# Kernel tuning notes

Measured on AMD Instinct MI355X. Metric: run time of the kernel, lower is better.

Reference implementation:

```python
import jax, jax.numpy as jnp
import numpy as np

B, T, C, H = 1, 4096, 768, 12
D = C // H  # head_dim = 64


def setup_inputs() -> dict:
    key = jax.random.key(0)
    ks = jax.random.split(key, 5)
    s = 1.0 / np.sqrt(C)
    return {
        "x": jax.random.normal(ks[0], (B, T, C), dtype=jnp.float32),
        "Wq": jax.random.normal(ks[1], (C, C), dtype=jnp.float32) * s,
        "bq": jnp.zeros((C,), dtype=jnp.float32),
        "Wk": jax.random.normal(ks[2], (C, C), dtype=jnp.float32) * s,
        "bk": jnp.zeros((C,), dtype=jnp.float32),
        "Wv": jax.random.normal(ks[3], (C, C), dtype=jnp.float32) * s,
        "bv": jnp.zeros((C,), dtype=jnp.float32),
        "Wo": jax.random.normal(ks[4], (C, C), dtype=jnp.float32) * s,
        "bo": jnp.zeros((C,), dtype=jnp.float32),
    }


def reference(x, Wq, bq, Wk, bk, Wv, bv, Wo, bo):
    # Linear projections (torch nn.Linear: y = x @ W.T + b)
    q = (x @ Wq.T + bq).reshape(B, T, H, D).transpose(0, 2, 1, 3)  # [B,H,T,D]
    k = (x @ Wk.T + bk).reshape(B, T, H, D).transpose(0, 2, 1, 3)
    v = (x @ Wv.T + bv).reshape(B, T, H, D).transpose(0, 2, 1, 3)
    scale = 1.0 / jnp.sqrt(jnp.asarray(D, dtype=x.dtype))
    scores = jnp.einsum("bhqd,bhkd->bhqk", q, k) * scale  # [B,H,T,T]
    attn = jax.nn.softmax(scores, axis=-1)
    out = jnp.einsum("bhqk,bhkd->bhqd", attn, v)  # [B,H,T,D]
    y = out.transpose(0, 2, 1, 3).reshape(B, T, C)
    return y @ Wo.T + bo
```

## Files before the change

### kernel.cpp

```cpp
#include <hip/hip_runtime.h>
#include <math.h>

#define T_ 4096
#define C_ 768
#define H_ 12
#define D_ 64
#define TC_ ((size_t)T_ * C_)
#define CC_ ((size_t)C_ * C_)

typedef __attribute__((ext_vector_type(8))) __bf16 bf16x8;
typedef __attribute__((ext_vector_type(4))) __bf16 bf16x4;
typedef __attribute__((ext_vector_type(2))) __bf16 bf16x2;
typedef __attribute__((ext_vector_type(4))) float f32x4;
typedef __attribute__((ext_vector_type(16))) float f32x16;
typedef __attribute__((ext_vector_type(8))) unsigned short u16x8;

#define MFIX 24.0f

static __device__ __forceinline__ float fast_exp2(float x) {
#if __has_builtin(__builtin_amdgcn_exp2f)
    return __builtin_amdgcn_exp2f(x);
#else
    return exp2f(x);
#endif
}

static __device__ __forceinline__ unsigned pack2(float a, float b) {
    bf16x2 v = { (__bf16)a, (__bf16)b };
    return __builtin_bit_cast(unsigned, v);
}

static __device__ __forceinline__ void gload16(const void* g, void* l) {
    __builtin_amdgcn_global_load_lds(
        (const __attribute__((address_space(1))) unsigned int*)g,
        (__attribute__((address_space(3))) unsigned int*)l, 16, 0, 0);
}

__global__ void f2b_kernel(const float* __restrict__ in,
                           unsigned short* __restrict__ out, int n4) {
    int i = blockIdx.x * blockDim.x + threadIdx.x;
    const int stride = gridDim.x * blockDim.x;
    for (; i < n4; i += stride) {
        float4 v = ((const float4*)in)[i];
        bf16x4 o = { (__bf16)v.x, (__bf16)v.y, (__bf16)v.z, (__bf16)v.w };
        *(bf16x4*)&out[(size_t)i * 4] = o;
    }
}

__global__ void f2b4_kernel(const float* __restrict__ w0, const float* __restrict__ w1,
                            const float* __restrict__ w2, const float* __restrict__ w3,
                            unsigned short* __restrict__ out) {
    const float* src = (blockIdx.y == 0) ? w0 : (blockIdx.y == 1) ? w1
                     : (blockIdx.y == 2) ? w2 : w3;
    unsigned short* dst = out + (size_t)blockIdx.y * CC_;
    const int i = blockIdx.x * blockDim.x + threadIdx.x;
    float4 v = ((const float4*)src)[i];
    bf16x4 o = { (__bf16)v.x, (__bf16)v.y, (__bf16)v.z, (__bf16)v.w };
    *(bf16x4*)&dst[(size_t)i * 4] = o;
}

#define BM 128
#define BN 128
#define BKG 64

struct GemmRegs {
    const unsigned short* ag[4];
    const unsigned short* wg[4];
    unsigned short* la[4];
    unsigned short* lw[4];
    int lq, lg, wr, wc;
};

static __device__ __forceinline__ void gemm_setup(
    GemmRegs& R, const unsigned short* A, const unsigned short* W,
    unsigned short* Asm, unsigned short* Bsm, int bm, int bn, int K)
{
    const int tid = threadIdx.x;
    const int wave = tid >> 6, lane = tid & 63;
    R.lq = lane & 15; R.lg = lane >> 4;
    R.wr = wave >> 1; R.wc = wave & 1;
#pragma unroll
    for (int i = 0; i < 4; ++i) {
        const int flat = wave * 256 + i * 64 + lane;
        const int row = flat >> 3, cb = flat & 7;
        R.ag[i] = A + (size_t)(bm + row) * K + cb * 8;
        R.wg[i] = W + (size_t)(bn + row) * K + cb * 8;
        R.la[i] = Asm + (wave * 4 + i) * 512;
        R.lw[i] = Bsm + (wave * 4 + i) * 512;
    }
}

static __device__ __forceinline__ void gemm_loop(
    GemmRegs& R, unsigned short* Asm, unsigned short* Bsm, int K, f32x4 acc[4][4])
{
    for (int kb = 0; kb < K; kb += BKG) {
        __syncthreads();
#pragma unroll
        for (int i = 0; i < 4; ++i) {
            gload16(R.ag[i] + kb, R.la[i]);
            gload16(R.wg[i] + kb, R.lw[i]);
        }
        __syncthreads();
        __builtin_amdgcn_s_setprio(1);
#pragma unroll
        for (int ks = 0; ks < 2; ++ks) {
            bf16x8 af[4], wf[4];
#pragma unroll
            for (int m = 0; m < 4; ++m)
                af[m] = *(const bf16x8*)&Asm[(R.wr * 64 + m * 16 + R.lq) * BKG + ks * 32 + R.lg * 8];
#pragma unroll
            for (int n = 0; n < 4; ++n)
                wf[n] = *(const bf16x8*)&Bsm[(R.wc * 64 + n * 16 + R.lq) * BKG + ks * 32 + R.lg * 8];
#pragma unroll
            for (int m = 0; m < 4; ++m)
#pragma unroll
                for (int n = 0; n < 4; ++n)
                    acc[m][n] = __builtin_amdgcn_mfma_f32_16x16x32_bf16(af[m], wf[n], acc[m][n], 0, 0, 0);
        }
        __builtin_amdgcn_s_setprio(0);
    }
}

__global__ __launch_bounds__(256) void qkv128(
    const unsigned short* __restrict__ xb,
    const unsigned short* __restrict__ Wqb, const unsigned short* __restrict__ Wkb,
    const unsigned short* __restrict__ Wvb,
    const float* __restrict__ bq, const float* __restrict__ bk, const float* __restrict__ bv,
    unsigned short* __restrict__ Qb, unsigned short* __restrict__ Kb,
    unsigned short* __restrict__ Vtb)
{
    __shared__ unsigned short Asm[BM * BKG];
    __shared__ unsigned short Bsm[BN * BKG];
    const int z = blockIdx.z;
    const unsigned short* W = (z == 0) ? Wqb : (z == 1) ? Wkb : Wvb;
    const float* bias = (z == 0) ? bq : (z == 1) ? bk : bv;
    const int bm = blockIdx.x * BM, bn = blockIdx.y * BN;

    GemmRegs R;
    gemm_setup(R, xb, W, Asm, Bsm, bm, bn, C_);
    f32x4 acc[4][4] = {};
    gemm_loop(R, Asm, Bsm, C_, acc);

    const float sc = (z == 0) ? 0.18033688011112042f : 1.0f;
#pragma unroll
    for (int mt = 0; mt < 4; ++mt) {
        const int m0 = bm + R.wr * 64 + mt * 16 + R.lg * 4;
#pragma unroll
        for (int nt = 0; nt < 4; ++nt) {
            const int n = bn + R.wc * 64 + nt * 16 + R.lq;
            const float b = bias[n];
            if (z == 2) {
                bf16x4 o = { (__bf16)(acc[mt][nt][0] + b), (__bf16)(acc[mt][nt][1] + b),
                             (__bf16)(acc[mt][nt][2] + b), (__bf16)(acc[mt][nt][3] + b) };
                *(bf16x4*)&Vtb[(size_t)n * T_ + m0] = o;
            } else {
                unsigned short* Y = (z == 0) ? Qb : Kb;
#pragma unroll
                for (int r = 0; r < 4; ++r)
                    Y[(size_t)(m0 + r) * C_ + n] =
                        __builtin_bit_cast(unsigned short, (__bf16)((acc[mt][nt][r] + b) * sc));
            }
        }
    }
}

__global__ __launch_bounds__(256) void out128(
    const unsigned short* __restrict__ ctxb, const unsigned short* __restrict__ Wob,
    const float* __restrict__ bo, float* __restrict__ out)
{
    __shared__ unsigned short Asm[BM * BKG];
    __shared__ unsigned short Bsm[BN * BKG];
    const int bm = blockIdx.x * BM, bn = blockIdx.y * BN;

    GemmRegs R;
    gemm_setup(R, ctxb, Wob, Asm, Bsm, bm, bn, C_);
    f32x4 acc[4][4] = {};
    gemm_loop(R, Asm, Bsm, C_, acc);

#pragma unroll
    for (int mt = 0; mt < 4; ++mt) {
        const int m0 = bm + R.wr * 64 + mt * 16 + R.lg * 4;
#pragma unroll
        for (int nt = 0; nt < 4; ++nt) {
            const int n = bn + R.wc * 64 + nt * 16 + R.lq;
            const float b = bo[n];
#pragma unroll
            for (int r = 0; r < 4; ++r)
                out[(size_t)(m0 + r) * C_ + n] = acc[mt][nt][r] + b;
        }
    }
}

#define SPLITS 2
#define KVTILES (T_ / 64 / SPLITS)

__global__ __launch_bounds__(128, 3) void attn32s(
    const unsigned short* __restrict__ Qb, const unsigned short* __restrict__ Kb,
    const unsigned short* __restrict__ Vtb, unsigned short* __restrict__ Opart,
    float* __restrict__ mlpart)
{
    __shared__ unsigned short Ks[64 * 64];
    __shared__ unsigned short Vs[64 * 64];
    __shared__ unsigned short Ps[2][32 * 64];

    const int tid = threadIdx.x;
    const int wave = tid >> 6, lane = tid & 63;
    const int lq = lane & 31, hi = lane >> 5;

    const int bid = blockIdx.x;
    const int sw = (bid & 7) * 192 + (bid >> 3);
    const int split = sw / 768;
    const int rem = sw - split * 768;
    const int h = rem >> 6, qt = rem & 63;
    const int q0 = qt * 64 + wave * 32;
    const int kv0 = split * (T_ / SPLITS);

    const int swz = (lq & 7) << 4;
    int rof[4];
#pragma unroll
    for (int ks = 0; ks < 4; ++ks)
        rof[ks] = lq * 128 + ((hi * 16 + ks * 32) ^ swz);

    bf16x8 qf[4];
    {
        const unsigned short* qp = Qb + (size_t)(q0 + lq) * C_ + h * D_ + hi * 8;
#pragma unroll
        for (int ks = 0; ks < 4; ++ks) qf[ks] = *(const bf16x8*)(qp + ks * 16);
    }

    const int srow = (lane >> 3);
    const int soff = (lane & 7) * 16;
    const char* gkb = (const char*)Kb +
        (size_t)(kv0 + wave * 32 + srow) * (C_ * 2) + h * (D_ * 2) + soff;
    const char* gvb = (const char*)Vtb +
        (size_t)(h * D_ + wave * 32 + srow) * (T_ * 2) + kv0 * 2 + soff;
    char* kds = (char*)Ks + (wave * 32 + srow) * 128 + (soff ^ (srow << 4));
    char* vds = (char*)Vs + (wave * 32 + srow) * 128 + (soff ^ (srow << 4));

    u16x8 kreg[4], vreg[4];
#pragma unroll
    for (int k = 0; k < 4; ++k) {
        kreg[k] = *(const u16x8*)(gkb + k * 8 * (C_ * 2));
        vreg[k] = *(const u16x8*)(gvb + k * 8 * (T_ * 2));
    }

    f32x16 oacc0 = {}, oacc1 = {};
    float lrun = 0.f;

    for (int it = 0; it < KVTILES; ++it) {
        __syncthreads();
#pragma unroll
        for (int k = 0; k < 4; ++k) {
            *(u16x8*)(kds + k * 1024) = kreg[k];
            *(u16x8*)(vds + k * 1024) = vreg[k];
        }
        __syncthreads();

        if (it + 1 < KVTILES) {
            const char* gk = gkb + (size_t)(it + 1) * 64 * (C_ * 2);
            const char* gv = gvb + (size_t)(it + 1) * 128;
#pragma unroll
            for (int k = 0; k < 4; ++k) {
                kreg[k] = *(const u16x8*)(gk + k * 8 * (C_ * 2));
                vreg[k] = *(const u16x8*)(gv + k * 8 * (T_ * 2));
            }
        }

        const char* kb = (const char*)&Ks[0];
        const char* vb = (const char*)&Vs[0];

        f32x16 s0 = {}, s1 = {};
        __builtin_amdgcn_s_setprio(1);
#pragma unroll
        for (int ks = 0; ks < 4; ++ks) {
            bf16x8 kf0 = *(const bf16x8*)(kb + rof[ks]);
            bf16x8 kf1 = *(const bf16x8*)(kb + 4096 + rof[ks]);
            s0 = __builtin_amdgcn_mfma_f32_32x32x16_bf16(kf0, qf[ks], s0, 0, 0, 0);
            s1 = __builtin_amdgcn_mfma_f32_32x32x16_bf16(kf1, qf[ks], s1, 0, 0, 0);
        }
        __builtin_amdgcn_s_setprio(0);

#pragma unroll
        for (int r = 0; r < 16; ++r) {
            s0[r] = fast_exp2(s0[r] - MFIX);
            s1[r] = fast_exp2(s1[r] - MFIX);
        }
        {
            float ps[8];
#pragma unroll
            for (int r = 0; r < 8; ++r)
                ps[r] = (s0[r] + s0[r + 8]) + (s1[r] + s1[r + 8]);
            ps[0] += ps[4]; ps[1] += ps[5]; ps[2] += ps[6]; ps[3] += ps[7];
            float pt = (ps[0] + ps[1]) + (ps[2] + ps[3]);
            lrun += pt + __shfl_xor(pt, 32);
        }

        char* pw = (char*)&Ps[wave][0] + lq * 128;
#pragma unroll
        for (int g = 0; g < 4; ++g) {
            uint2 w0 = { pack2(s0[4 * g + 0], s0[4 * g + 1]),
                         pack2(s0[4 * g + 2], s0[4 * g + 3]) };
            *(uint2*)(pw + ((16 * g) ^ swz) + 8 * hi) = w0;
            uint2 w1 = { pack2(s1[4 * g + 0], s1[4 * g + 1]),
                         pack2(s1[4 * g + 2], s1[4 * g + 3]) };
            *(uint2*)(pw + ((16 * (g + 4)) ^ swz) + 8 * hi) = w1;
        }

        __builtin_amdgcn_s_setprio(1);
#pragma unroll
        for (int ks = 0; ks < 4; ++ks) {
            bf16x8 pf = *(const bf16x8*)((const char*)&Ps[wave][0] + lq * 128 +
                                         (((unsigned)(ks * 32 + hi * 16)) ^ swz));
            bf16x8 vf0 = *(const bf16x8*)(vb + rof[ks]);
            bf16x8 vf1 = *(const bf16x8*)(vb + 4096 + rof[ks]);
            oacc0 = __builtin_amdgcn_mfma_f32_32x32x16_bf16(vf0, pf, oacc0, 0, 0, 0);
            oacc1 = __builtin_amdgcn_mfma_f32_32x32x16_bf16(vf1, pf, oacc1, 0, 0, 0);
        }
        __builtin_amdgcn_s_setprio(0);
    }

    unsigned short* op = Opart + ((size_t)(split * H_ + h) * T_ + q0 + lq) * 64;
#pragma unroll
    for (int k = 0; k < 4; ++k) {
        bf16x4 o0 = { (__bf16)oacc0[4 * k + 0], (__bf16)oacc0[4 * k + 1],
                      (__bf16)oacc0[4 * k + 2], (__bf16)oacc0[4 * k + 3] };
        *(bf16x4*)&op[8 * k + 4 * hi] = o0;
        bf16x4 o1 = { (__bf16)oacc1[4 * k + 0], (__bf16)oacc1[4 * k + 1],
                      (__bf16)oacc1[4 * k + 2], (__bf16)oacc1[4 * k + 3] };
        *(bf16x4*)&op[32 + 8 * k + 4 * hi] = o1;
    }
    if (hi == 0) {
        float2 ml; ml.x = MFIX; ml.y = lrun;
        *(float2*)&mlpart[((size_t)(split * H_ + h) * T_ + q0 + lq) * 2] = ml;
    }
}

__global__ __launch_bounds__(256) void combine2(
    const unsigned short* __restrict__ Opart, const float* __restrict__ mlpart,
    unsigned short* __restrict__ ctxb)
{
    const int idx = blockIdx.x * 256 + threadIdx.x;
    const int dq = idx & 15;
    const int ht = idx >> 4;
    const int h = ht >> 12;
    const int t = ht & (T_ - 1);
    const size_t b0 = (size_t)h * T_ + t;
    const size_t b1 = (size_t)(H_ + h) * T_ + t;
    const float2 ml0 = *(const float2*)&mlpart[b0 * 2];
    const float2 ml1 = *(const float2*)&mlpart[b1 * 2];
    const float m = fmaxf(ml0.x, ml1.x);
    const float w0 = fast_exp2(ml0.x - m);
    const float w1 = fast_exp2(ml1.x - m);
    const float inv = 1.f / (w0 * ml0.y + w1 * ml1.y);
    const bf16x4 a0 = *(const bf16x4*)&Opart[b0 * 64 + dq * 4];
    const bf16x4 a1 = *(const bf16x4*)&Opart[b1 * 64 + dq * 4];
    bf16x4 r;
#pragma unroll
    for (int i = 0; i < 4; ++i)
        r[i] = (__bf16)(((float)a0[i] * w0 + (float)a1[i] * w1) * inv);
    *(bf16x4*)&ctxb[(size_t)t * C_ + h * D_ + dq * 4] = r;
}

extern "C" void kernel_launch(void* const* d_in, const int* in_sizes, int n_in,
                              void* d_out, int out_size, void* d_ws, size_t ws_size,
                              hipStream_t stream) {
    (void)in_sizes; (void)n_in; (void)out_size; (void)ws_size;
    const float* x  = (const float*)d_in[0];
    const float* Wq = (const float*)d_in[1];
    const float* bq = (const float*)d_in[2];
    const float* Wk = (const float*)d_in[3];
    const float* bk = (const float*)d_in[4];
    const float* Wv = (const float*)d_in[5];
    const float* bv = (const float*)d_in[6];
    const float* Wo = (const float*)d_in[7];
    const float* bo = (const float*)d_in[8];
    float* out = (float*)d_out;

    unsigned short* ws    = (unsigned short*)d_ws;
    unsigned short* xb    = ws;
    unsigned short* Wqb   = xb + TC_;
    unsigned short* Wkb   = Wqb + CC_;
    unsigned short* Wvb   = Wkb + CC_;
    unsigned short* Wob   = Wvb + CC_;
    unsigned short* Qb    = Wob + CC_;
    unsigned short* Kb    = Qb + TC_;
    unsigned short* Vtb   = Kb + TC_;
    unsigned short* ctxb  = Vtb + TC_;
    unsigned short* Opart = ctxb + TC_;
    float* mlpart = (float*)(Opart + 2 * TC_);

    f2b_kernel<<<2048, 256, 0, stream>>>(x, xb, (int)(TC_ / 4));
    dim3 gw(CC_ / 4 / 256, 4);
    f2b4_kernel<<<gw, 256, 0, stream>>>(Wq, Wk, Wv, Wo, Wqb);

    dim3 gq(T_ / BM, C_ / BN, 3);
    qkv128<<<gq, 256, 0, stream>>>(xb, Wqb, Wkb, Wvb, bq, bk, bv, Qb, Kb, Vtb);

    attn32s<<<1536, 128, 0, stream>>>(Qb, Kb, Vtb, Opart, mlpart);
    combine2<<<(T_ * H_ * 16) / 256, 256, 0, stream>>>(Opart, mlpart, ctxb);

    dim3 go(T_ / BM, C_ / BN);
    out128<<<go, 256, 0, stream>>>(ctxb, Wob, bo, out);
}
```

Measured before the change: 140.2 us.

## Keep P in registers via lane shuffles and raise attention KV splits to four

The softmax probabilities are repacked into MFMA B-operand fragments with cross-half lane shuffles instead of a round trip through LDS. This drops the Ps shared buffer and raises the occupancy hint from 3 to 5 blocks. The KV dimension is now split four ways when the workspace is large enough, which doubles the grid to 3072 blocks. The combine step sums the split partials directly, since all splits share the fixed max. The extra split adds more partial-output traffic to and from global memory in the combine kernel.

```diff
diff --git a/kernel.cpp b/kernel.cpp
--- a/kernel.cpp
+++ b/kernel.cpp
@@ -14,6 +14,7 @@
 typedef __attribute__((ext_vector_type(4))) float f32x4;
 typedef __attribute__((ext_vector_type(16))) float f32x16;
 typedef __attribute__((ext_vector_type(8))) unsigned short u16x8;
+typedef __attribute__((ext_vector_type(4))) unsigned int u32x4;
 
 #define MFIX 24.0f
 
@@ -191,29 +192,28 @@
     }
 }
 
-#define SPLITS 2
-#define KVTILES (T_ / 64 / SPLITS)
-
-__global__ __launch_bounds__(128, 3) void attn32s(
+template <int SPLITS>
+__global__ __launch_bounds__(128, 5) void attn32s(
     const unsigned short* __restrict__ Qb, const unsigned short* __restrict__ Kb,
     const unsigned short* __restrict__ Vtb, unsigned short* __restrict__ Opart,
-    float* __restrict__ mlpart)
+    float* __restrict__ lpart)
 {
     __shared__ unsigned short Ks[64 * 64];
     __shared__ unsigned short Vs[64 * 64];
-    __shared__ unsigned short Ps[2][32 * 64];
 
     const int tid = threadIdx.x;
     const int wave = tid >> 6, lane = tid & 63;
     const int lq = lane & 31, hi = lane >> 5;
 
+    const int perx = (SPLITS * 768) / 8;
     const int bid = blockIdx.x;
-    const int sw = (bid & 7) * 192 + (bid >> 3);
+    const int sw = (bid & 7) * perx + (bid >> 3);
     const int split = sw / 768;
     const int rem = sw - split * 768;
     const int h = rem >> 6, qt = rem & 63;
     const int q0 = qt * 64 + wave * 32;
     const int kv0 = split * (T_ / SPLITS);
+    const int KVTILES = T_ / 64 / SPLITS;
 
     const int swz = (lq & 7) << 4;
     int rof[4];
@@ -295,26 +295,36 @@
             lrun += pt + __shfl_xor(pt, 32);
         }
 
-        char* pw = (char*)&Ps[wave][0] + lq * 128;
-#pragma unroll
-        for (int g = 0; g < 4; ++g) {
-            uint2 w0 = { pack2(s0[4 * g + 0], s0[4 * g + 1]),
-                         pack2(s0[4 * g + 2], s0[4 * g + 3]) };
-            *(uint2*)(pw + ((16 * g) ^ swz) + 8 * hi) = w0;
-            uint2 w1 = { pack2(s1[4 * g + 0], s1[4 * g + 1]),
-                         pack2(s1[4 * g + 2], s1[4 * g + 3]) };
-            *(uint2*)(pw + ((16 * (g + 4)) ^ swz) + 8 * hi) = w1;
+        bf16x8 pf[4];
+#pragma unroll
+        for (int half = 0; half < 2; ++half) {
+            const f32x16& s = half ? s1 : s0;
+            unsigned g[8];
+#pragma unroll
+            for (int a = 0; a < 8; ++a) g[a] = pack2(s[2 * a], s[2 * a + 1]);
+            unsigned V0 = hi ? g[0] : g[2];
+            unsigned V1 = hi ? g[1] : g[3];
+            unsigned xV0 = __shfl_xor((int)V0, 32);
+            unsigned xV1 = __shfl_xor((int)V1, 32);
+            u32x4 pk0 = { hi ? xV0 : g[0], hi ? xV1 : g[1],
+                          hi ? g[2] : xV0, hi ? g[3] : xV1 };
+            pf[2 * half + 0] = __builtin_bit_cast(bf16x8, pk0);
+            unsigned W0 = hi ? g[4] : g[6];
+            unsigned W1 = hi ? g[5] : g[7];
+            unsigned xW0 = __shfl_xor((int)W0, 32);
+            unsigned xW1 = __shfl_xor((int)W1, 32);
+            u32x4 pk1 = { hi ? xW0 : g[4], hi ? xW1 : g[5],
+                          hi ? g[6] : xW0, hi ? g[7] : xW1 };
+            pf[2 * half + 1] = __builtin_bit_cast(bf16x8, pk1);
         }
 
         __builtin_amdgcn_s_setprio(1);
 #pragma unroll
         for (int ks = 0; ks < 4; ++ks) {
-            bf16x8 pf = *(const bf16x8*)((const char*)&Ps[wave][0] + lq * 128 +
-                                         (((unsigned)(ks * 32 + hi * 16)) ^ swz));
             bf16x8 vf0 = *(const bf16x8*)(vb + rof[ks]);
             bf16x8 vf1 = *(const bf16x8*)(vb + 4096 + rof[ks]);
-            oacc0 = __builtin_amdgcn_mfma_f32_32x32x16_bf16(vf0, pf, oacc0, 0, 0, 0);
-            oacc1 = __builtin_amdgcn_mfma_f32_32x32x16_bf16(vf1, pf, oacc1, 0, 0, 0);
+            oacc0 = __builtin_amdgcn_mfma_f32_32x32x16_bf16(vf0, pf[ks], oacc0, 0, 0, 0);
+            oacc1 = __builtin_amdgcn_mfma_f32_32x32x16_bf16(vf1, pf[ks], oacc1, 0, 0, 0);
         }
         __builtin_amdgcn_s_setprio(0);
     }
@@ -329,14 +339,13 @@
                       (__bf16)oacc1[4 * k + 2], (__bf16)oacc1[4 * k + 3] };
         *(bf16x4*)&op[32 + 8 * k + 4 * hi] = o1;
     }
-    if (hi == 0) {
-        float2 ml; ml.x = MFIX; ml.y = lrun;
-        *(float2*)&mlpart[((size_t)(split * H_ + h) * T_ + q0 + lq) * 2] = ml;
-    }
-}
-
-__global__ __launch_bounds__(256) void combine2(
-    const unsigned short* __restrict__ Opart, const float* __restrict__ mlpart,
+    if (hi == 0)
+        lpart[(size_t)(split * H_ + h) * T_ + q0 + lq] = lrun;
+}
+
+template <int SPLITS>
+__global__ __launch_bounds__(256) void combineS(
+    const unsigned short* __restrict__ Opart, const float* __restrict__ lpart,
     unsigned short* __restrict__ ctxb)
 {
     const int idx = blockIdx.x * 256 + threadIdx.x;
@@ -344,27 +353,30 @@
     const int ht = idx >> 4;
     const int h = ht >> 12;
     const int t = ht & (T_ - 1);
-    const size_t b0 = (size_t)h * T_ + t;
-    const size_t b1 = (size_t)(H_ + h) * T_ + t;
-    const float2 ml0 = *(const float2*)&mlpart[b0 * 2];
-    const float2 ml1 = *(const float2*)&mlpart[b1 * 2];
-    const float m = fmaxf(ml0.x, ml1.x);
-    const float w0 = fast_exp2(ml0.x - m);
-    const float w1 = fast_exp2(ml1.x - m);
-    const float inv = 1.f / (w0 * ml0.y + w1 * ml1.y);
-    const bf16x4 a0 = *(const bf16x4*)&Opart[b0 * 64 + dq * 4];
-    const bf16x4 a1 = *(const bf16x4*)&Opart[b1 * 64 + dq * 4];
+
+    float denom = 0.f;
+#pragma unroll
+    for (int sp = 0; sp < SPLITS; ++sp)
+        denom += lpart[(size_t)(sp * H_ + h) * T_ + t];
+    const float inv = 1.f / denom;
+
+    float acc[4] = {};
+#pragma unroll
+    for (int sp = 0; sp < SPLITS; ++sp) {
+        const bf16x4 a = *(const bf16x4*)&Opart[((size_t)(sp * H_ + h) * T_ + t) * 64 + dq * 4];
+#pragma unroll
+        for (int i = 0; i < 4; ++i) acc[i] += (float)a[i];
+    }
     bf16x4 r;
 #pragma unroll
-    for (int i = 0; i < 4; ++i)
-        r[i] = (__bf16)(((float)a0[i] * w0 + (float)a1[i] * w1) * inv);
+    for (int i = 0; i < 4; ++i) r[i] = (__bf16)(acc[i] * inv);
     *(bf16x4*)&ctxb[(size_t)t * C_ + h * D_ + dq * 4] = r;
 }
 
 extern "C" void kernel_launch(void* const* d_in, const int* in_sizes, int n_in,
                               void* d_out, int out_size, void* d_ws, size_t ws_size,
                               hipStream_t stream) {
-    (void)in_sizes; (void)n_in; (void)out_size; (void)ws_size;
+    (void)in_sizes; (void)n_in; (void)out_size;
     const float* x  = (const float*)d_in[0];
     const float* Wq = (const float*)d_in[1];
     const float* bq = (const float*)d_in[2];
@@ -387,7 +399,10 @@
     unsigned short* Vtb   = Kb + TC_;
     unsigned short* ctxb  = Vtb + TC_;
     unsigned short* Opart = ctxb + TC_;
-    float* mlpart = (float*)(Opart + 2 * TC_);
+
+    const size_t lsz = (size_t)H_ * T_ * sizeof(float);
+    const size_t need4 = (size_t)(9 * TC_ + 4 * CC_) * 2 + 4 * lsz;
+    const int S = (ws_size >= need4) ? 4 : 2;
 
     f2b_kernel<<<2048, 256, 0, stream>>>(x, xb, (int)(TC_ / 4));
     dim3 gw(CC_ / 4 / 256, 4);
@@ -396,8 +411,15 @@
     dim3 gq(T_ / BM, C_ / BN, 3);
     qkv128<<<gq, 256, 0, stream>>>(xb, Wqb, Wkb, Wvb, bq, bk, bv, Qb, Kb, Vtb);
 
-    attn32s<<<1536, 128, 0, stream>>>(Qb, Kb, Vtb, Opart, mlpart);
-    combine2<<<(T_ * H_ * 16) / 256, 256, 0, stream>>>(Opart, mlpart, ctxb);
+    if (S == 4) {
+        float* lpart = (float*)(Opart + 4 * TC_);
+        attn32s<4><<<4 * 768, 128, 0, stream>>>(Qb, Kb, Vtb, Opart, lpart);
+        combineS<4><<<(T_ * H_ * 16) / 256, 256, 0, stream>>>(Opart, lpart, ctxb);
+    } else {
+        float* lpart = (float*)(Opart + 2 * TC_);
+        attn32s<2><<<2 * 768, 128, 0, stream>>>(Qb, Kb, Vtb, Opart, lpart);
+        combineS<2><<<(T_ * H_ * 16) / 256, 256, 0, stream>>>(Opart, lpart, ctxb);
+    }
 
     dim3 go(T_ / BM, C_ / BN);
     out128<<<go, 256, 0, stream>>>(ctxb, Wob, bo, out);
```

After: 291.3 us. 108% more time.
